# Kernel optimization log

Measured on AMD Instinct MI355X. Metric: run time of the kernel, lower is better.

Reference implementation:

```python
import jax, jax.numpy as jnp
import numpy as np

C_LEN, Q_LEN, B, H = 2048, 512, 32, 256


def setup_inputs() -> dict:
    key = jax.random.key(0)
    k1, k2 = jax.random.split(key)
    content_vec = jax.random.normal(k1, (C_LEN, B, H), dtype=jnp.float32)
    question_vec = jax.random.normal(k2, (Q_LEN, B, H), dtype=jnp.float32)
    question_mask = jnp.ones((B, Q_LEN), dtype=jnp.int32)
    return {"content_vec": content_vec, "question_vec": question_vec, "question_mask": question_mask}


def reference(content_vec, question_vec, question_mask):
    # scores: (B, c_len, q_len) = content (b,c,h) @ question^T (b,h,q)
    scores = jnp.einsum('cbh,qbh->bcq', content_vec, question_vec)
    # additive -inf mask where question_mask == 0, broadcast over c_len
    neg_inf = jnp.asarray(-jnp.inf, dtype=scores.dtype)
    scores = jnp.where(question_mask[:, None, :] == 0, neg_inf, scores)
    attn = jax.nn.softmax(scores, axis=-1)  # (B, c_len, q_len)
    # weighted sum of question vectors -> back to (c_len, B, H)
    out = jnp.einsum('bcq,qbh->cbh', attn, question_vec)
    return out
```

## Files before the change

### kernel.cpp

```cpp
#include <hip/hip_runtime.h>

#define C_LENX 2048
#define Q_LENX 512
#define BATCH  32
#define HDIM   256
#define BH     8192
#define CBLK   128
#define QBLK   32
#define NQT    16
#define TILE_BYTES 32768
#define OFF_QT 16384

typedef __attribute__((ext_vector_type(8))) _Float16 f16x8;
typedef __attribute__((ext_vector_type(4))) _Float16 f16x4;
typedef __attribute__((ext_vector_type(4))) float f32x4;

__device__ __forceinline__ unsigned short f2h_bits(float x) {
    union { _Float16 h; unsigned short u; } cv;
    cv.h = (_Float16)x;
    return cv.u;
}

__device__ __forceinline__ void stage16(const void* gsrc, void* ldst) {
    __builtin_amdgcn_global_load_lds(
        (const __attribute__((address_space(1))) unsigned int*)gsrc,
        (__attribute__((address_space(3))) unsigned int*)ldst, 16, 0, 0);
}

__global__ __launch_bounds__(256)
void q_prep(const float* __restrict__ question, unsigned char* __restrict__ blob)
{
    __shared__ unsigned short sHf[QBLK][264];
    const int tid = threadIdx.x;
    const int b  = blockIdx.x >> 4;
    const int t  = blockIdx.x & 15;
    const float* qbase = question + (size_t)(t * QBLK) * BH + b * HDIM;
    unsigned char* tb = blob + (size_t)(b * NQT + t) * TILE_BYTES;

    #pragma unroll
    for (int i = 0; i < 8; ++i) {
        int e  = tid + i * 256;
        int qr = e >> 6;
        int h4 = (e & 63) << 2;
        float4 x = *reinterpret_cast<const float4*>(qbase + (size_t)qr * BH + h4);
        ushort4 hv;
        hv.x = f2h_bits(x.x); hv.y = f2h_bits(x.y);
        hv.z = f2h_bits(x.z); hv.w = f2h_bits(x.w);
        *reinterpret_cast<ushort4*>(&sHf[qr][h4]) = hv;
        int c = h4 >> 3;
        *reinterpret_cast<ushort4*>(tb + qr * 512 + ((c ^ (qr & 7)) << 4) + ((h4 & 7) << 1)) = hv;
    }
    __syncthreads();
    #pragma unroll
    for (int i = 0; i < 4; ++i) {
        int e  = tid + i * 256;
        int h  = e >> 2;
        int g  = e & 3;
        int q0 = g * 8;
        ushort4 a, bv;
        a.x  = sHf[q0 + 0][h]; a.y  = sHf[q0 + 1][h];
        a.z  = sHf[q0 + 2][h]; a.w  = sHf[q0 + 3][h];
        bv.x = sHf[q0 + 4][h]; bv.y = sHf[q0 + 5][h];
        bv.z = sHf[q0 + 6][h]; bv.w = sHf[q0 + 7][h];
        *reinterpret_cast<ushort4*>(tb + OFF_QT + e * 16)     = a;
        *reinterpret_cast<ushort4*>(tb + OFF_QT + e * 16 + 8) = bv;
    }
}

__global__ __launch_bounds__(256, 2)
void s2s_attn(const float* __restrict__ content,
              const unsigned char* __restrict__ blob,
              const int*   __restrict__ qmask,
              float*       __restrict__ out)
{
    __shared__ __attribute__((aligned(16))) unsigned char sBuf[2 * TILE_BYTES];
    __shared__ __attribute__((aligned(16))) unsigned short sP[2][4][16][40];

    const int tid  = threadIdx.x;
    const int wid  = tid >> 6;
    const int lane = tid & 63;
    const int lr   = lane & 15;
    const int lg   = lane >> 4;

    const int lin = (blockIdx.x & 7) * 64 + (blockIdx.x >> 3);
    const int ct = lin & 15;
    const int b  = lin >> 4;
    const int c0 = ct * CBLK;

    {
        const unsigned char* tb0 = blob + (size_t)(b * NQT) * TILE_BYTES;
        #pragma unroll
        for (int j = 0; j < 8; ++j) {
            int seg = wid * 8 + j;
            stage16(tb0 + seg * 1024 + lane * 16, sBuf + seg * 1024);
        }
    }

    unsigned mwv[NQT];
    #pragma unroll
    for (int t = 0; t < NQT; ++t)
        mwv[t] = (unsigned)__ballot(qmask[b * Q_LENX + t * QBLK + (lane & 31)] != 0);

    f16x8 chi0[8], chi1[8];
    {
        const float* cb0 = content + (size_t)(c0 + wid*16 + lr) * BH + b*HDIM + lg*8;
        const float* cb1 = cb0 + (size_t)64 * BH;
        #pragma unroll
        for (int kc = 0; kc < 8; ++kc) {
            float4 x0 = *reinterpret_cast<const float4*>(cb0 + kc*32);
            float4 x1 = *reinterpret_cast<const float4*>(cb0 + kc*32 + 4);
            float4 y0 = *reinterpret_cast<const float4*>(cb1 + kc*32);
            float4 y1 = *reinterpret_cast<const float4*>(cb1 + kc*32 + 4);
            float xs[8] = {x0.x,x0.y,x0.z,x0.w,x1.x,x1.y,x1.z,x1.w};
            float ys[8] = {y0.x,y0.y,y0.z,y0.w,y1.x,y1.y,y1.z,y1.w};
            #pragma unroll
            for (int j = 0; j < 8; ++j) {
                chi0[kc][j] = (_Float16)xs[j];
                chi1[kc][j] = (_Float16)ys[j];
            }
        }
    }

    f32x4 acc0[16], acc1[16];
    #pragma unroll
    for (int n = 0; n < 16; ++n) {
        f32x4 z = {0.f,0.f,0.f,0.f};
        acc0[n] = z; acc1[n] = z;
    }
    float m_run0 = -INFINITY, m_run1 = -INFINITY;
    float l_run0 = 0.f, l_run1 = 0.f;

    __syncthreads();

    for (int t = 0; t < NQT; ++t) {
        const unsigned char* qf = sBuf + (t & 1) * TILE_BYTES;
        const unsigned char* qt = qf + OFF_QT;

        if (t + 1 < NQT) {
            const unsigned char* tbn = blob + (size_t)(b * NQT + t + 1) * TILE_BYTES;
            unsigned char* db = sBuf + ((t + 1) & 1) * TILE_BYTES;
            #pragma unroll
            for (int j = 0; j < 8; ++j) {
                int seg = wid * 8 + j;
                stage16(tbn + seg * 1024 + lane * 16, db + seg * 1024);
            }
        }
        const unsigned mw = mwv[t];

        f32x4 zz = {0.f,0.f,0.f,0.f};
        f32x4 sA0=zz, sB0=zz, sA1=zz, sB1=zz;
        const unsigned swz = (unsigned)(lr & 7);
        __builtin_amdgcn_s_setprio(1);
        #pragma unroll
        for (int kc = 0; kc < 8; ++kc) {
            unsigned off = (unsigned)((kc*4 + lg) ^ swz) << 4;
            f16x8 qa = *reinterpret_cast<const f16x8*>(qf + lr*512 + off);
            f16x8 qb = *reinterpret_cast<const f16x8*>(qf + (16+lr)*512 + off);
            sA0 = __builtin_amdgcn_mfma_f32_16x16x32_f16(qa, chi0[kc], sA0, 0, 0, 0);
            sB0 = __builtin_amdgcn_mfma_f32_16x16x32_f16(qb, chi0[kc], sB0, 0, 0, 0);
            sA1 = __builtin_amdgcn_mfma_f32_16x16x32_f16(qa, chi1[kc], sA1, 0, 0, 0);
            sB1 = __builtin_amdgcn_mfma_f32_16x16x32_f16(qb, chi1[kc], sB1, 0, 0, 0);
        }
        __builtin_amdgcn_s_setprio(0);

        float p0v[8], p1v[8];
        float tm0 = -INFINITY, tm1 = -INFINITY;
        if (mw == 0xffffffffu) {
            #pragma unroll
            for (int r = 0; r < 4; ++r) {
                p0v[r] = sA0[r]; p0v[4+r] = sB0[r];
                p1v[r] = sA1[r]; p1v[4+r] = sB1[r];
                tm0 = fmaxf(tm0, fmaxf(sA0[r], sB0[r]));
                tm1 = fmaxf(tm1, fmaxf(sA1[r], sB1[r]));
            }
        } else {
            #pragma unroll
            for (int r = 0; r < 4; ++r) {
                bool okA = (mw >> (lg*4 + r)) & 1u;
                bool okB = (mw >> (16 + lg*4 + r)) & 1u;
                float a0 = okA ? sA0[r] : -INFINITY;
                float b0v = okB ? sB0[r] : -INFINITY;
                float a1 = okA ? sA1[r] : -INFINITY;
                float b1v = okB ? sB1[r] : -INFINITY;
                p0v[r] = a0; p0v[4+r] = b0v;
                p1v[r] = a1; p1v[4+r] = b1v;
                tm0 = fmaxf(tm0, fmaxf(a0, b0v));
                tm1 = fmaxf(tm1, fmaxf(a1, b1v));
            }
        }
        tm0 = fmaxf(tm0, __shfl_xor(tm0, 16, 64));
        tm0 = fmaxf(tm0, __shfl_xor(tm0, 32, 64));
        tm1 = fmaxf(tm1, __shfl_xor(tm1, 16, 64));
        tm1 = fmaxf(tm1, __shfl_xor(tm1, 32, 64));

        if (__ballot((tm0 > m_run0 + 4.0f) || (tm1 > m_run1 + 4.0f))) {
            float mn0 = fmaxf(m_run0, tm0);
            float mn1 = fmaxf(m_run1, tm1);
            float sc0 = 1.f, sc1 = 1.f;
            if (mn0 != -INFINITY) { sc0 = __expf(m_run0 - mn0); m_run0 = mn0; }
            if (mn1 != -INFINITY) { sc1 = __expf(m_run1 - mn1); m_run1 = mn1; }
            l_run0 *= sc0; l_run1 *= sc1;
            #pragma unroll
            for (int n = 0; n < 16; ++n) {
                acc0[n] *= sc0;
                acc1[n] *= sc1;
            }
        }

        _Float16 ph0[8], ph1[8];
        {
            float ps0 = 0.f, ps1 = 0.f;
            if (m_run0 == -INFINITY) {
                #pragma unroll
                for (int i = 0; i < 8; ++i) ph0[i] = (_Float16)0.f;
            } else {
                #pragma unroll
                for (int i = 0; i < 8; ++i) {
                    float e = __expf(p0v[i] - m_run0);
                    ph0[i] = (_Float16)e;
                    ps0 += (float)ph0[i];
                }
            }
            if (m_run1 == -INFINITY) {
                #pragma unroll
                for (int i = 0; i < 8; ++i) ph1[i] = (_Float16)0.f;
            } else {
                #pragma unroll
                for (int i = 0; i < 8; ++i) {
                    float e = __expf(p1v[i] - m_run1);
                    ph1[i] = (_Float16)e;
                    ps1 += (float)ph1[i];
                }
            }
            l_run0 += ps0;
            l_run1 += ps1;
        }

        {
            f16x4 w00 = {ph0[0], ph0[1], ph0[2], ph0[3]};
            f16x4 w01 = {ph0[4], ph0[5], ph0[6], ph0[7]};
            f16x4 w10 = {ph1[0], ph1[1], ph1[2], ph1[3]};
            f16x4 w11 = {ph1[4], ph1[5], ph1[6], ph1[7]};
            *reinterpret_cast<f16x4*>(&sP[0][wid][lr][lg*4])      = w00;
            *reinterpret_cast<f16x4*>(&sP[0][wid][lr][16 + lg*4]) = w01;
            *reinterpret_cast<f16x4*>(&sP[1][wid][lr][lg*4])      = w10;
            *reinterpret_cast<f16x4*>(&sP[1][wid][lr][16 + lg*4]) = w11;
        }
        asm volatile("s_waitcnt lgkmcnt(0)" ::: "memory");
        __builtin_amdgcn_sched_barrier(0);
        f16x8 pf0 = *reinterpret_cast<const f16x8*>(&sP[0][wid][lr][lg*8]);
        f16x8 pf1 = *reinterpret_cast<const f16x8*>(&sP[1][wid][lr][lg*8]);

        __builtin_amdgcn_s_setprio(1);
        #pragma unroll
        for (int n = 0; n < 16; ++n) {
            f16x8 vt = *reinterpret_cast<const f16x8*>(qt + (((n*16 + lr)*4 + lg) << 4));
            acc0[n] = __builtin_amdgcn_mfma_f32_16x16x32_f16(vt, pf0, acc0[n], 0, 0, 0);
            acc1[n] = __builtin_amdgcn_mfma_f32_16x16x32_f16(vt, pf1, acc1[n], 0, 0, 0);
        }
        __builtin_amdgcn_s_setprio(0);

        __syncthreads();
    }

    l_run0 += __shfl_xor(l_run0, 16, 64);
    l_run0 += __shfl_xor(l_run0, 32, 64);
    l_run1 += __shfl_xor(l_run1, 16, 64);
    l_run1 += __shfl_xor(l_run1, 32, 64);
    float rinv0 = 1.f / l_run0;
    float rinv1 = 1.f / l_run1;
    float* orow0 = out + (size_t)(c0 + wid*16 + lr) * BH + b*HDIM;
    float* orow1 = orow0 + (size_t)64 * BH;
    #pragma unroll
    for (int n = 0; n < 16; ++n) {
        f32x4 v0 = acc0[n] * rinv0;
        f32x4 v1 = acc1[n] * rinv1;
        *reinterpret_cast<f32x4*>(orow0 + n*16 + lg*4) = v0;
        *reinterpret_cast<f32x4*>(orow1 + n*16 + lg*4) = v1;
    }
}

extern "C" void kernel_launch(void* const* d_in, const int* in_sizes, int n_in,
                              void* d_out, int out_size, void* d_ws, size_t ws_size,
                              hipStream_t stream) {
    const float* content  = (const float*)d_in[0];
    const float* question = (const float*)d_in[1];
    const int*   mask     = (const int*)d_in[2];
    float*       out      = (float*)d_out;

    unsigned char* blob = (unsigned char*)d_ws;

    q_prep<<<BATCH * NQT, 256, 0, stream>>>(question, blob);
    s2s_attn<<<C_LENX / CBLK * BATCH, 256, 0, stream>>>(content, blob, mask, out);
}
```

Measured before the change: 75.23 us.

## Read Q tiles straight from global into registers instead of LDS staging

```diff
diff --git a/kernel.cpp b/kernel.cpp
--- a/kernel.cpp
+++ b/kernel.cpp
@@ -19,12 +19,6 @@
     union { _Float16 h; unsigned short u; } cv;
     cv.h = (_Float16)x;
     return cv.u;
-}
-
-__device__ __forceinline__ void stage16(const void* gsrc, void* ldst) {
-    __builtin_amdgcn_global_load_lds(
-        (const __attribute__((address_space(1))) unsigned int*)gsrc,
-        (__attribute__((address_space(3))) unsigned int*)ldst, 16, 0, 0);
 }
 
 __global__ __launch_bounds__(256)
@@ -73,7 +67,6 @@
               const int*   __restrict__ qmask,
               float*       __restrict__ out)
 {
-    __shared__ __attribute__((aligned(16))) unsigned char sBuf[2 * TILE_BYTES];
     __shared__ __attribute__((aligned(16))) unsigned short sP[2][4][16][40];
 
     const int tid  = threadIdx.x;
@@ -86,15 +79,6 @@
     const int ct = lin & 15;
     const int b  = lin >> 4;
     const int c0 = ct * CBLK;
-
-    {
-        const unsigned char* tb0 = blob + (size_t)(b * NQT) * TILE_BYTES;
-        #pragma unroll
-        for (int j = 0; j < 8; ++j) {
-            int seg = wid * 8 + j;
-            stage16(tb0 + seg * 1024 + lane * 16, sBuf + seg * 1024);
-        }
-    }
 
     unsigned mwv[NQT];
     #pragma unroll
@@ -130,36 +114,34 @@
     float m_run0 = -INFINITY, m_run1 = -INFINITY;
     float l_run0 = 0.f, l_run1 = 0.f;
 
-    __syncthreads();
+    const unsigned swz = (unsigned)(lr & 7);
 
     for (int t = 0; t < NQT; ++t) {
-        const unsigned char* qf = sBuf + (t & 1) * TILE_BYTES;
+        const unsigned char* qf = blob + (size_t)(b * NQT + t) * TILE_BYTES;
         const unsigned char* qt = qf + OFF_QT;
-
-        if (t + 1 < NQT) {
-            const unsigned char* tbn = blob + (size_t)(b * NQT + t + 1) * TILE_BYTES;
-            unsigned char* db = sBuf + ((t + 1) & 1) * TILE_BYTES;
-            #pragma unroll
-            for (int j = 0; j < 8; ++j) {
-                int seg = wid * 8 + j;
-                stage16(tbn + seg * 1024 + lane * 16, db + seg * 1024);
-            }
-        }
         const unsigned mw = mwv[t];
+
+        f16x8 qfr[16];
+        #pragma unroll
+        for (int kc = 0; kc < 8; ++kc) {
+            unsigned off = (unsigned)((kc*4 + lg) ^ swz) << 4;
+            qfr[2*kc]   = *reinterpret_cast<const f16x8*>(qf + lr*512 + off);
+            qfr[2*kc+1] = *reinterpret_cast<const f16x8*>(qf + (16+lr)*512 + off);
+        }
+        f16x8 vt0[8];
+        #pragma unroll
+        for (int n = 0; n < 8; ++n)
+            vt0[n] = *reinterpret_cast<const f16x8*>(qt + (((n*16 + lr)*4 + lg) << 4));
 
         f32x4 zz = {0.f,0.f,0.f,0.f};
         f32x4 sA0=zz, sB0=zz, sA1=zz, sB1=zz;
-        const unsigned swz = (unsigned)(lr & 7);
         __builtin_amdgcn_s_setprio(1);
         #pragma unroll
         for (int kc = 0; kc < 8; ++kc) {
-            unsigned off = (unsigned)((kc*4 + lg) ^ swz) << 4;
-            f16x8 qa = *reinterpret_cast<const f16x8*>(qf + lr*512 + off);
-            f16x8 qb = *reinterpret_cast<const f16x8*>(qf + (16+lr)*512 + off);
-            sA0 = __builtin_amdgcn_mfma_f32_16x16x32_f16(qa, chi0[kc], sA0, 0, 0, 0);
-            sB0 = __builtin_amdgcn_mfma_f32_16x16x32_f16(qb, chi0[kc], sB0, 0, 0, 0);
-            sA1 = __builtin_amdgcn_mfma_f32_16x16x32_f16(qa, chi1[kc], sA1, 0, 0, 0);
-            sB1 = __builtin_amdgcn_mfma_f32_16x16x32_f16(qb, chi1[kc], sB1, 0, 0, 0);
+            sA0 = __builtin_amdgcn_mfma_f32_16x16x32_f16(qfr[2*kc],   chi0[kc], sA0, 0, 0, 0);
+            sB0 = __builtin_amdgcn_mfma_f32_16x16x32_f16(qfr[2*kc+1], chi0[kc], sB0, 0, 0, 0);
+            sA1 = __builtin_amdgcn_mfma_f32_16x16x32_f16(qfr[2*kc],   chi1[kc], sA1, 0, 0, 0);
+            sB1 = __builtin_amdgcn_mfma_f32_16x16x32_f16(qfr[2*kc+1], chi1[kc], sB1, 0, 0, 0);
         }
         __builtin_amdgcn_s_setprio(0);
 
@@ -251,16 +233,23 @@
         f16x8 pf0 = *reinterpret_cast<const f16x8*>(&sP[0][wid][lr][lg*8]);
         f16x8 pf1 = *reinterpret_cast<const f16x8*>(&sP[1][wid][lr][lg*8]);
 
+        f16x8 vt1[8];
+        #pragma unroll
+        for (int n = 0; n < 8; ++n)
+            vt1[n] = *reinterpret_cast<const f16x8*>(qt + ((((n+8)*16 + lr)*4 + lg) << 4));
+
         __builtin_amdgcn_s_setprio(1);
         #pragma unroll
-        for (int n = 0; n < 16; ++n) {
-            f16x8 vt = *reinterpret_cast<const f16x8*>(qt + (((n*16 + lr)*4 + lg) << 4));
-            acc0[n] = __builtin_amdgcn_mfma_f32_16x16x32_f16(vt, pf0, acc0[n], 0, 0, 0);
-            acc1[n] = __builtin_amdgcn_mfma_f32_16x16x32_f16(vt, pf1, acc1[n], 0, 0, 0);
+        for (int n = 0; n < 8; ++n) {
+            acc0[n] = __builtin_amdgcn_mfma_f32_16x16x32_f16(vt0[n], pf0, acc0[n], 0, 0, 0);
+            acc1[n] = __builtin_amdgcn_mfma_f32_16x16x32_f16(vt0[n], pf1, acc1[n], 0, 0, 0);
+        }
+        #pragma unroll
+        for (int n = 0; n < 8; ++n) {
+            acc0[8+n] = __builtin_amdgcn_mfma_f32_16x16x32_f16(vt1[n], pf0, acc0[8+n], 0, 0, 0);
+            acc1[8+n] = __builtin_amdgcn_mfma_f32_16x16x32_f16(vt1[n], pf1, acc1[8+n], 0, 0, 0);
         }
         __builtin_amdgcn_s_setprio(0);
-
-        __syncthreads();
     }
 
     l_run0 += __shfl_xor(l_run0, 16, 64);
```

New measurement: 192.4 us. 2.56x slower.

## Permute transposed Q layout to consume softmax probabilities directly from registers

Applied to the files above, without the earlier changes.

```diff
diff --git a/kernel.cpp b/kernel.cpp
--- a/kernel.cpp
+++ b/kernel.cpp
@@ -12,7 +12,6 @@
 #define OFF_QT 16384
 
 typedef __attribute__((ext_vector_type(8))) _Float16 f16x8;
-typedef __attribute__((ext_vector_type(4))) _Float16 f16x4;
 typedef __attribute__((ext_vector_type(4))) float f32x4;
 
 __device__ __forceinline__ unsigned short f2h_bits(float x) {
@@ -56,12 +55,12 @@
         int e  = tid + i * 256;
         int h  = e >> 2;
         int g  = e & 3;
-        int q0 = g * 8;
+        int q0 = g * 4;
         ushort4 a, bv;
-        a.x  = sHf[q0 + 0][h]; a.y  = sHf[q0 + 1][h];
-        a.z  = sHf[q0 + 2][h]; a.w  = sHf[q0 + 3][h];
-        bv.x = sHf[q0 + 4][h]; bv.y = sHf[q0 + 5][h];
-        bv.z = sHf[q0 + 6][h]; bv.w = sHf[q0 + 7][h];
+        a.x  = sHf[q0 + 0][h];      a.y  = sHf[q0 + 1][h];
+        a.z  = sHf[q0 + 2][h];      a.w  = sHf[q0 + 3][h];
+        bv.x = sHf[16 + q0 + 0][h]; bv.y = sHf[16 + q0 + 1][h];
+        bv.z = sHf[16 + q0 + 2][h]; bv.w = sHf[16 + q0 + 3][h];
         *reinterpret_cast<ushort4*>(tb + OFF_QT + e * 16)     = a;
         *reinterpret_cast<ushort4*>(tb + OFF_QT + e * 16 + 8) = bv;
     }
@@ -74,7 +73,6 @@
               float*       __restrict__ out)
 {
     __shared__ __attribute__((aligned(16))) unsigned char sBuf[2 * TILE_BYTES];
-    __shared__ __attribute__((aligned(16))) unsigned short sP[2][4][16][40];
 
     const int tid  = threadIdx.x;
     const int wid  = tid >> 6;
@@ -207,6 +205,13 @@
             }
         }
 
+        f16x8 vt0[8], vt1[8];
+        #pragma unroll
+        for (int n = 0; n < 8; ++n) {
+            vt0[n] = *reinterpret_cast<const f16x8*>(qt + (((n*16 + lr)*4 + lg) << 4));
+            vt1[n] = *reinterpret_cast<const f16x8*>(qt + ((((n+8)*16 + lr)*4 + lg) << 4));
+        }
+
         _Float16 ph0[8], ph1[8];
         {
             float ps0 = 0.f, ps1 = 0.f;
@@ -236,27 +241,19 @@
             l_run1 += ps1;
         }
 
-        {
-            f16x4 w00 = {ph0[0], ph0[1], ph0[2], ph0[3]};
-            f16x4 w01 = {ph0[4], ph0[5], ph0[6], ph0[7]};
-            f16x4 w10 = {ph1[0], ph1[1], ph1[2], ph1[3]};
-            f16x4 w11 = {ph1[4], ph1[5], ph1[6], ph1[7]};
-            *reinterpret_cast<f16x4*>(&sP[0][wid][lr][lg*4])      = w00;
-            *reinterpret_cast<f16x4*>(&sP[0][wid][lr][16 + lg*4]) = w01;
-            *reinterpret_cast<f16x4*>(&sP[1][wid][lr][lg*4])      = w10;
-            *reinterpret_cast<f16x4*>(&sP[1][wid][lr][16 + lg*4]) = w11;
-        }
-        asm volatile("s_waitcnt lgkmcnt(0)" ::: "memory");
-        __builtin_amdgcn_sched_barrier(0);
-        f16x8 pf0 = *reinterpret_cast<const f16x8*>(&sP[0][wid][lr][lg*8]);
-        f16x8 pf1 = *reinterpret_cast<const f16x8*>(&sP[1][wid][lr][lg*8]);
+        f16x8 pf0 = {ph0[0], ph0[1], ph0[2], ph0[3], ph0[4], ph0[5], ph0[6], ph0[7]};
+        f16x8 pf1 = {ph1[0], ph1[1], ph1[2], ph1[3], ph1[4], ph1[5], ph1[6], ph1[7]};
 
         __builtin_amdgcn_s_setprio(1);
         #pragma unroll
-        for (int n = 0; n < 16; ++n) {
-            f16x8 vt = *reinterpret_cast<const f16x8*>(qt + (((n*16 + lr)*4 + lg) << 4));
-            acc0[n] = __builtin_amdgcn_mfma_f32_16x16x32_f16(vt, pf0, acc0[n], 0, 0, 0);
-            acc1[n] = __builtin_amdgcn_mfma_f32_16x16x32_f16(vt, pf1, acc1[n], 0, 0, 0);
+        for (int n = 0; n < 8; ++n) {
+            acc0[n] = __builtin_amdgcn_mfma_f32_16x16x32_f16(vt0[n], pf0, acc0[n], 0, 0, 0);
+            acc1[n] = __builtin_amdgcn_mfma_f32_16x16x32_f16(vt0[n], pf1, acc1[n], 0, 0, 0);
+        }
+        #pragma unroll
+        for (int n = 0; n < 8; ++n) {
+            acc0[8+n] = __builtin_amdgcn_mfma_f32_16x16x32_f16(vt1[n], pf0, acc0[8+n], 0, 0, 0);
+            acc1[8+n] = __builtin_amdgcn_mfma_f32_16x16x32_f16(vt1[n], pf1, acc1[8+n], 0, 0, 0);
         }
         __builtin_amdgcn_s_setprio(0);
 
```

New measurement: 109.6 us. 45.7% more time.
